# Optimization experiments

Measured on AMD Instinct MI355X. Metric: run time of the kernel, lower is better.

The kernel has to match this reference:

```python
import jax, jax.numpy as jnp
import numpy as np

D_MODEL = 2048
N_HEADS = 16
N_KV = 8
HEAD_DIM = 128
G = N_HEADS // N_KV  # q heads per kv head
SCALE = float(np.sqrt(HEAD_DIM))
B, T = 2, 2048


def setup_inputs() -> dict:
    key = jax.random.key(0)
    k1, k2, k3, k4, k5 = jax.random.split(key, 5)
    s = 0.02
    return {
        "x": jax.random.normal(k1, (B, T, D_MODEL), dtype=jnp.float32),
        "Wq": jax.random.normal(k2, (N_HEADS * HEAD_DIM, D_MODEL), dtype=jnp.float32) * s,
        "Wk": jax.random.normal(k3, (N_KV * HEAD_DIM, D_MODEL), dtype=jnp.float32) * s,
        "Wv": jax.random.normal(k4, (N_KV * HEAD_DIM, D_MODEL), dtype=jnp.float32) * s,
        "Wo": jax.random.normal(k5, (D_MODEL, N_HEADS * HEAD_DIM), dtype=jnp.float32) * s,
    }


def reference(x, Wq, Wk, Wv, Wo):
    # Projections (nn.Linear: y = x @ W.T), dropout prob = 0 so omitted.
    b, t, _ = x.shape
    q = (x @ Wq.T).reshape(b, t, N_KV, G, HEAD_DIM)   # (B,T,Hkv,G,d)
    k = (x @ Wk.T).reshape(b, t, N_KV, HEAD_DIM)      # (B,T,Hkv,d)
    v = (x @ Wv.T).reshape(b, t, N_KV, HEAD_DIM)
    # GQA: each kv head shared by G query heads (equivalent to repeat_interleave).
    scores = jnp.einsum('btghd,bsgd->bghts', q, k) / SCALE  # (B,Hkv,G,T,T)
    attn = jax.nn.softmax(scores, axis=-1)
    out = jnp.einsum('bghts,bsgd->btghd', attn, v)          # (B,T,Hkv,G,d)
    out = out.reshape(b, t, N_HEADS * HEAD_DIM)
    return out @ Wo.T
```

## Files before the change

### kernel.cpp

```cpp
#include <hip/hip_runtime.h>
#include <hip/hip_bf16.h>

typedef __attribute__((ext_vector_type(8))) short short8;
typedef __attribute__((ext_vector_type(4))) float floatx4;

__device__ inline unsigned short f2bf(float f) {
    unsigned int u = __float_as_uint(f);
    u += 0x7fffu + ((u >> 16) & 1u);
    return (unsigned short)(u >> 16);
}

__device__ inline unsigned int pk_bf16(float lo, float hi) {
    __hip_bfloat162 h = __float22bfloat162_rn(float2{lo, hi});
    unsigned int u;
    __builtin_memcpy(&u, &h, 4);
    return u;
}

__global__ void cast_all_kernel(const float* __restrict__ x,
                                const float* __restrict__ wq,
                                const float* __restrict__ wk,
                                const float* __restrict__ wv,
                                const float* __restrict__ wo,
                                unsigned short* __restrict__ xb,
                                unsigned short* __restrict__ wqkb,
                                unsigned short* __restrict__ wvb,
                                unsigned short* __restrict__ wob) {
    const float C2 = 0.08838834764831845f * 1.4426950408889634f;
    int bid = blockIdx.x;
    const float* src;
    unsigned short* dst;
    int base;
    float sc = 1.0f;
    if (bid < 8192)       { src = x;  dst = xb;             base = bid; }
    else if (bid < 12288) { src = wq; dst = wqkb;           base = bid - 8192; sc = C2; }
    else if (bid < 14336) { src = wk; dst = wqkb + 4194304; base = bid - 12288; }
    else if (bid < 16384) { src = wv; dst = wvb;            base = bid - 14336; }
    else                  { src = wo; dst = wob;            base = bid - 16384; }
    int i = base * 256 + threadIdx.x;
    float4 v = ((const float4*)src)[i];
    ushort4 o;
    o.x = f2bf(v.x * sc); o.y = f2bf(v.y * sc);
    o.z = f2bf(v.z * sc); o.w = f2bf(v.w * sc);
    ((ushort4*)dst)[i] = o;
}

template <int OUT_BF16>
__device__ __forceinline__ void gemm256_body(
        const unsigned short* __restrict__ A,
        const unsigned short* __restrict__ B,
        void* __restrict__ Cp, int ldc, int m0, int n0,
        unsigned short* sL) {
    const int tid  = threadIdx.x;
    const int wave = tid >> 6;
    const int lane = tid & 63;
    const int l16  = lane & 15;
    const int lq   = lane >> 4;
    const int wm   = (wave >> 2) * 128;
    const int wn   = (wave & 3) * 64;
    const int kx   = lq ^ (l16 & 3);

    floatx4 acc[8][4] = {};

    const unsigned short* gA[2];
    const unsigned short* gB[2];
#pragma unroll
    for (int i = 0; i < 2; i++) {
        int c   = wave * 2 + i;
        int row = c * 16 + (lane >> 2);
        int g   = (lane & 3) ^ (row & 3);
        gA[i] = A + (size_t)(m0 + row) * 2048 + g * 8;
        gB[i] = B + (size_t)(n0 + row) * 2048 + g * 8;
    }

#define STG_A32(slot)                                                          \
    do {                                                                       \
        _Pragma("unroll")                                                      \
        for (int i = 0; i < 2; i++) {                                          \
            __builtin_amdgcn_global_load_lds(                                  \
                (const __attribute__((address_space(1))) void*)gA[i],          \
                (__attribute__((address_space(3))) void*)(sL + (slot) * 16384 +\
                                                          (wave * 2 + i) * 512),\
                16, 0, 0);                                                     \
            gA[i] += 32;                                                       \
        }                                                                      \
    } while (0)
#define STG_B32(slot)                                                          \
    do {                                                                       \
        _Pragma("unroll")                                                      \
        for (int i = 0; i < 2; i++) {                                          \
            __builtin_amdgcn_global_load_lds(                                  \
                (const __attribute__((address_space(1))) void*)gB[i],          \
                (__attribute__((address_space(3))) void*)(sL + (slot) * 16384 +\
                                                  8192 + (wave * 2 + i) * 512),\
                16, 0, 0);                                                     \
            gB[i] += 32;                                                       \
        }                                                                      \
    } while (0)

    STG_A32(0); STG_B32(0);
    STG_A32(1); STG_B32(1);

    for (int t = 0; t < 64; t++) {
        const int sc = t & 3;
        const int sn = (t + 2) & 3;
        if (t < 63) asm volatile("s_waitcnt vmcnt(4)" ::: "memory");
        else        asm volatile("s_waitcnt vmcnt(0)" ::: "memory");
        __builtin_amdgcn_s_barrier();
        asm volatile("" ::: "memory");

        const unsigned short* sAc = sL + sc * 16384;
        const unsigned short* sBc = sAc + 8192;
        short8 af[4], bf[4];

#pragma unroll
        for (int mb = 0; mb < 4; mb++)
            af[mb] = *(const short8*)(sAc + (wm + mb * 16 + l16) * 32 + kx * 8);
#pragma unroll
        for (int nb = 0; nb < 4; nb++)
            bf[nb] = *(const short8*)(sBc + (wn + nb * 16 + l16) * 32 + kx * 8);
        if (t < 62) STG_A32(sn);
        __builtin_amdgcn_s_barrier();
        asm volatile("s_waitcnt lgkmcnt(0)" ::: "memory");
        __builtin_amdgcn_sched_barrier(0);
        __builtin_amdgcn_s_setprio(1);
#pragma unroll
        for (int mb = 0; mb < 4; mb++)
#pragma unroll
            for (int nb = 0; nb < 4; nb++)
                acc[mb][nb] = __builtin_amdgcn_mfma_f32_16x16x32_bf16(
                    af[mb], bf[nb], acc[mb][nb], 0, 0, 0);
        __builtin_amdgcn_s_setprio(0);
        __builtin_amdgcn_s_barrier();
        asm volatile("" ::: "memory");

#pragma unroll
        for (int mb = 0; mb < 4; mb++)
            af[mb] = *(const short8*)(sAc + (wm + 64 + mb * 16 + l16) * 32 + kx * 8);
        if (t < 62) STG_B32(sn);
        __builtin_amdgcn_s_barrier();
        asm volatile("s_waitcnt lgkmcnt(0)" ::: "memory");
        __builtin_amdgcn_sched_barrier(0);
        __builtin_amdgcn_s_setprio(1);
#pragma unroll
        for (int mb = 0; mb < 4; mb++)
#pragma unroll
            for (int nb = 0; nb < 4; nb++)
                acc[4 + mb][nb] = __builtin_amdgcn_mfma_f32_16x16x32_bf16(
                    af[mb], bf[nb], acc[4 + mb][nb], 0, 0, 0);
        __builtin_amdgcn_s_setprio(0);
    }
#undef STG_A32
#undef STG_B32

#pragma unroll
    for (int mb = 0; mb < 8; mb++)
#pragma unroll
        for (int nb = 0; nb < 4; nb++)
#pragma unroll
            for (int r = 0; r < 4; r++) {
                int row = m0 + wm + mb * 16 + lq * 4 + r;
                int col = n0 + wn + nb * 16 + l16;
                if (OUT_BF16)
                    ((unsigned short*)Cp)[(size_t)row * ldc + col] = f2bf(acc[mb][nb][r]);
                else
                    ((float*)Cp)[(size_t)row * ldc + col] = acc[mb][nb][r];
            }
}

__global__ __launch_bounds__(512, 1) void gemm_qkv_kernel(
        const unsigned short* __restrict__ x_bf,
        const unsigned short* __restrict__ Wqk,
        const unsigned short* __restrict__ Wv,
        unsigned short* __restrict__ QKb,
        unsigned short* __restrict__ Vtb) {
    __shared__ __align__(16) unsigned short sL[4 * 16384];
    const int bid = blockIdx.x;
    if (bid < 192) {
        gemm256_body<1>(x_bf, Wqk, QKb, 3072,
                        (bid / 12) * 256, (bid % 12) * 256, sL);
    } else {
        int t = bid - 192;
        gemm256_body<1>(Wv, x_bf, Vtb, 4096,
                        (t / 16) * 256, (t % 16) * 256, sL);
    }
}

template <int OUT_BF16>
__device__ __forceinline__ void gemm_bt64_body(
        const unsigned short* __restrict__ A,
        const unsigned short* __restrict__ B,
        void* __restrict__ Cp, int K, int ldc, int m0, int n0,
        unsigned short* sA, unsigned short* sB) {
    const int tid  = threadIdx.x;
    const int wave = tid >> 6;
    const int lane = tid & 63;
    const int l16  = lane & 15;
    const int lq   = lane >> 4;
    const int wm   = (wave >> 1) * 64;
    const int wn   = (wave & 1) * 64;

    floatx4 acc[4][4] = {};

    const unsigned short* gA[4];
    const unsigned short* gB[4];
#pragma unroll
    for (int i = 0; i < 4; i++) {
        int c   = wave * 4 + i;
        int row = c * 8 + (lane >> 3);
        int chs = (lane & 7) ^ (row & 7);
        gA[i] = A + (size_t)(m0 + row) * K + chs * 8;
        gB[i] = B + (size_t)(n0 + row) * K + chs * 8;
    }

    for (int k0 = 0; k0 < K; k0 += 64) {
        __syncthreads();
#pragma unroll
        for (int i = 0; i < 4; i++) {
            int c = wave * 4 + i;
            __builtin_amdgcn_global_load_lds(
                (const __attribute__((address_space(1))) void*)gA[i],
                (__attribute__((address_space(3))) void*)(sA + c * 512), 16, 0, 0);
            gA[i] += 64;
            __builtin_amdgcn_global_load_lds(
                (const __attribute__((address_space(1))) void*)gB[i],
                (__attribute__((address_space(3))) void*)(sB + c * 512), 16, 0, 0);
            gB[i] += 64;
        }
        __syncthreads();

        short8 af[2][4], bfr[2][4];
#pragma unroll
        for (int ks = 0; ks < 2; ks++) {
            int slot = (ks * 4 + lq) ^ (l16 & 7);
#pragma unroll
            for (int mb = 0; mb < 4; mb++)
                af[ks][mb] = *(const short8*)(sA + (wm + mb * 16 + l16) * 64 + slot * 8);
#pragma unroll
            for (int nb = 0; nb < 4; nb++)
                bfr[ks][nb] = *(const short8*)(sB + (wn + nb * 16 + l16) * 64 + slot * 8);
        }
#pragma unroll
        for (int ks = 0; ks < 2; ks++)
#pragma unroll
            for (int mb = 0; mb < 4; mb++)
#pragma unroll
                for (int nb = 0; nb < 4; nb++)
                    acc[mb][nb] = __builtin_amdgcn_mfma_f32_16x16x32_bf16(
                        af[ks][mb], bfr[ks][nb], acc[mb][nb], 0, 0, 0);
    }

#pragma unroll
    for (int mb = 0; mb < 4; mb++)
#pragma unroll
        for (int nb = 0; nb < 4; nb++)
#pragma unroll
            for (int r = 0; r < 4; r++) {
                int row = m0 + wm + mb * 16 + lq * 4 + r;
                int col = n0 + wn + nb * 16 + l16;
                if (OUT_BF16)
                    ((unsigned short*)Cp)[(size_t)row * ldc + col] = f2bf(acc[mb][nb][r]);
                else
                    ((float*)Cp)[(size_t)row * ldc + col] = acc[mb][nb][r];
            }
}

__global__ __launch_bounds__(256) void gemm_o_kernel(
        const unsigned short* __restrict__ A,
        const unsigned short* __restrict__ B,
        float* __restrict__ C) {
    __shared__ __align__(16) unsigned short sA[128 * 64];
    __shared__ __align__(16) unsigned short sB[128 * 64];
    gemm_bt64_body<0>(A, B, C, 2048, 2048,
                      blockIdx.y * 128, blockIdx.x * 128, sA, sB);
}

__global__ __launch_bounds__(256, 2) void flash_kernel(
        const unsigned short* __restrict__ QK,
        const unsigned short* __restrict__ Vt,
        unsigned short* __restrict__ O) {
    __shared__ __align__(16) unsigned short smem[40960];

    const int tid  = threadIdx.x;
    const int wave = tid >> 6;
    const int lane = tid & 63;
    const int l16  = lane & 15;
    const int lq   = lane >> 4;
    const int qt   = blockIdx.x;
    const int bh   = blockIdx.y;
    const int b    = bh >> 4;
    const int h    = bh & 15;
    const int kvh  = h >> 1;
    const size_t tokbase = (size_t)b * 2048 + qt * 128 + wave * 32;

    short8 qf[2][4];
#pragma unroll
    for (int qb = 0; qb < 2; qb++) {
        const unsigned short* qp =
            QK + (tokbase + qb * 16 + l16) * 3072 + h * 128 + lq * 8;
#pragma unroll
        for (int c = 0; c < 4; c++) qf[qb][c] = *(const short8*)(qp + c * 32);
    }

    const unsigned short* gKe =
        QK + ((size_t)b * 2048 + wave * 16 + lq) * 3072 + 2048 + kvh * 128 +
        (l16 ^ lq) * 8;
    const unsigned short* gKo =
        QK + ((size_t)b * 2048 + wave * 16 + 4 + lq) * 3072 + 2048 + kvh * 128 +
        (l16 ^ (lq + 4)) * 8;
    const unsigned short* gV0 =
        Vt + (size_t)(kvh * 128 + wave * 32 + (lane >> 3)) * 4096 +
        (size_t)b * 2048 + ((lane & 7) ^ (lane >> 3)) * 8;

#define STAGE_KT(sKd, sVd)                                                     \
    do {                                                                       \
        _Pragma("unroll")                                                      \
        for (int i = 0; i < 4; i++) {                                          \
            const unsigned short* gk =                                         \
                ((i & 1) ? gKo : gKe) + (i >> 1) * 24576;                      \
            __builtin_amdgcn_global_load_lds(                                  \
                (const __attribute__((address_space(1))) void*)gk,             \
                (__attribute__((address_space(3))) void*)((sKd) +              \
                                                          (wave * 4 + i) * 512),\
                16, 0, 0);                                                     \
            __builtin_amdgcn_global_load_lds(                                  \
                (const __attribute__((address_space(1))) void*)(gV0 +          \
                                                               i * 32768),     \
                (__attribute__((address_space(3))) void*)((sVd) +              \
                                                          (wave * 4 + i) * 512),\
                16, 0, 0);                                                     \
        }                                                                      \
        gKe += 196608; gKo += 196608; gV0 += 64;                               \
    } while (0)

    unsigned short* pB = smem + 32768 + wave * 2048;

    floatx4 oacc[2][8] = {};
    float l_run[2] = {0.0f, 0.0f};

    STAGE_KT(smem, smem + 16384);
    asm volatile("s_waitcnt vmcnt(0)" ::: "memory");
    __builtin_amdgcn_s_barrier();
    asm volatile("" ::: "memory");

    for (int kt = 0; kt < 32; kt++) {
        const int cur = kt & 1;
        const unsigned short* sKc = smem + cur * 8192;
        const unsigned short* sVc = smem + 16384 + cur * 8192;
        if (kt < 31) {
            unsigned short* sKn = smem + (cur ^ 1) * 8192;
            unsigned short* sVn = smem + 16384 + (cur ^ 1) * 8192;
            STAGE_KT(sKn, sVn);
        }

#pragma unroll
        for (int kb = 0; kb < 2; kb++) {
            floatx4 sacc[2] = {};
#pragma unroll
            for (int c = 0; c < 4; c++) {
                short8 kf = *(const short8*)(
                    sKc + (kb * 16 + l16) * 128 + (((c * 4 + lq) ^ (l16 & 7)) * 8));
#pragma unroll
                for (int qb = 0; qb < 2; qb++)
                    sacc[qb] = __builtin_amdgcn_mfma_f32_16x16x32_bf16(
                        kf, qf[qb][c], sacc[qb], 0, 0, 0);
            }
#pragma unroll
            for (int qb = 0; qb < 2; qb++) {
                float p0 = __builtin_exp2f(sacc[qb][0]);
                float p1 = __builtin_exp2f(sacc[qb][1]);
                float p2 = __builtin_exp2f(sacc[qb][2]);
                float p3 = __builtin_exp2f(sacc[qb][3]);
                l_run[qb] += (p0 + p1) + (p2 + p3);
                int row = qb * 16 + l16;
                uint2 u;
                u.x = pk_bf16(p0, p1);
                u.y = pk_bf16(p2, p3);
                *(uint2*)(pB + row * 64 +
                          (((kb * 2 + (lq >> 1)) ^ (row & 7)) * 8) +
                          (lq & 1) * 4) = u;
            }
        }
        asm volatile("s_waitcnt lgkmcnt(0)" ::: "memory");

        short8 pf0[2];
#pragma unroll
        for (int qb = 0; qb < 2; qb++) {
            int row = qb * 16 + l16;
            pf0[qb] = *(const short8*)(pB + row * 64 +
                                       ((lq ^ (row & 7)) * 8));
        }

        __builtin_amdgcn_s_setprio(1);
#pragma unroll
        for (int nb = 0; nb < 8; nb++) {
            short8 vf = *(const short8*)(
                sVc + (nb * 16 + l16) * 64 + ((lq ^ (l16 & 7)) * 8));
#pragma unroll
            for (int qb = 0; qb < 2; qb++)
                oacc[qb][nb] = __builtin_amdgcn_mfma_f32_16x16x32_bf16(
                    vf, pf0[qb], oacc[qb][nb], 0, 0, 0);
        }
        __builtin_amdgcn_s_setprio(0);

#pragma unroll
        for (int kb = 2; kb < 4; kb++) {
            floatx4 sacc[2] = {};
#pragma unroll
            for (int c = 0; c < 4; c++) {
                short8 kf = *(const short8*)(
                    sKc + (kb * 16 + l16) * 128 + (((c * 4 + lq) ^ (l16 & 7)) * 8));
#pragma unroll
                for (int qb = 0; qb < 2; qb++)
                    sacc[qb] = __builtin_amdgcn_mfma_f32_16x16x32_bf16(
                        kf, qf[qb][c], sacc[qb], 0, 0, 0);
            }
#pragma unroll
            for (int qb = 0; qb < 2; qb++) {
                float p0 = __builtin_exp2f(sacc[qb][0]);
                float p1 = __builtin_exp2f(sacc[qb][1]);
                float p2 = __builtin_exp2f(sacc[qb][2]);
                float p3 = __builtin_exp2f(sacc[qb][3]);
                l_run[qb] += (p0 + p1) + (p2 + p3);
                int row = qb * 16 + l16;
                uint2 u;
                u.x = pk_bf16(p0, p1);
                u.y = pk_bf16(p2, p3);
                *(uint2*)(pB + row * 64 +
                          (((kb * 2 + (lq >> 1)) ^ (row & 7)) * 8) +
                          (lq & 1) * 4) = u;
            }
        }
        asm volatile("s_waitcnt lgkmcnt(0)" ::: "memory");

        short8 pf1[2];
#pragma unroll
        for (int qb = 0; qb < 2; qb++) {
            int row = qb * 16 + l16;
            pf1[qb] = *(const short8*)(pB + row * 64 +
                                       (((4 + lq) ^ (row & 7)) * 8));
        }

        __builtin_amdgcn_s_setprio(1);
#pragma unroll
        for (int nb = 0; nb < 8; nb++) {
            short8 vf = *(const short8*)(
                sVc + (nb * 16 + l16) * 64 + (((4 + lq) ^ (l16 & 7)) * 8));
#pragma unroll
            for (int qb = 0; qb < 2; qb++)
                oacc[qb][nb] = __builtin_amdgcn_mfma_f32_16x16x32_bf16(
                    vf, pf1[qb], oacc[qb][nb], 0, 0, 0);
        }
        __builtin_amdgcn_s_setprio(0);

        asm volatile("s_waitcnt vmcnt(0)" ::: "memory");
        __builtin_amdgcn_s_barrier();
        asm volatile("" ::: "memory");
    }
#undef STAGE_KT

#pragma unroll
    for (int qb = 0; qb < 2; qb++) {
        float l = l_run[qb];
        l += __shfl_xor(l, 16);
        l += __shfl_xor(l, 32);
        float inv = 1.0f / l;
        size_t row = (tokbase + qb * 16 + l16) * 2048 + h * 128;
#pragma unroll
        for (int nb = 0; nb < 8; nb++) {
            uint2 u;
            u.x = pk_bf16(oacc[qb][nb][0] * inv, oacc[qb][nb][1] * inv);
            u.y = pk_bf16(oacc[qb][nb][2] * inv, oacc[qb][nb][3] * inv);
            *(uint2*)(O + row + nb * 16 + lq * 4) = u;
        }
    }
}

extern "C" void kernel_launch(void* const* d_in, const int* in_sizes, int n_in,
                              void* d_out, int out_size, void* d_ws, size_t ws_size,
                              hipStream_t stream) {
    const float* x  = (const float*)d_in[0];
    const float* Wq = (const float*)d_in[1];
    const float* Wk = (const float*)d_in[2];
    const float* Wv = (const float*)d_in[3];
    const float* Wo = (const float*)d_in[4];

    char* ws = (char*)d_ws;
    unsigned short* x_bf   = (unsigned short*)(ws);
    unsigned short* Wqk_bf = (unsigned short*)(ws + 16777216);
    unsigned short* Wv_bf  = (unsigned short*)(ws + 29360128);
    unsigned short* Wo_bf  = (unsigned short*)(ws + 33554432);
    unsigned short* QKb    = (unsigned short*)(ws + 41943040);
    unsigned short* Vtb    = (unsigned short*)(ws + 67108864);
    unsigned short* Ob     = (unsigned short*)(ws + 75497472);

    cast_all_kernel<<<dim3(20480), 256, 0, stream>>>(
        x, Wq, Wk, Wv, Wo, x_bf, Wqk_bf, Wv_bf, Wo_bf);

    gemm_qkv_kernel<<<dim3(256), 512, 0, stream>>>(x_bf, Wqk_bf, Wv_bf, QKb, Vtb);

    flash_kernel<<<dim3(16, 32), 256, 0, stream>>>(QKb, Vtb, Ob);

    gemm_o_kernel<<<dim3(16, 32), 256, 0, stream>>>(Ob, Wo_bf, (float*)d_out);
}
```

Measured before the change: 316.4 us.

## Rewrite output projection GEMM with 128x256 tiles and 4-stage async LDS pipeline

Replaces the output-projection GEMM body, which was single-buffered with two __syncthreads per 64-wide K step, with a 512-thread 128x256-tile kernel. The new body streams K in chunks of 32 through a 4-slot LDS ring using global_load_lds, issues loads two stages ahead, and waits with explicit vmcnt and s_barrier. It also raises MFMA priority with setprio. The aim is to hide global-load latency and raise MFMA utilisation. The cost is fewer blocks (256) at one block per CU and more intricate synchronisation.

Result: no change. 310.7 us, median of 2 (-1.8%).

```diff
diff --git a/kernel.cpp b/kernel.cpp
--- a/kernel.cpp
+++ b/kernel.cpp
@@ -168,6 +168,106 @@
             }
 }
 
+template <int OUT_BF16>
+__device__ __forceinline__ void gemm128_body(
+        const unsigned short* __restrict__ A,
+        const unsigned short* __restrict__ B,
+        void* __restrict__ Cp, int ldc, int m0, int n0,
+        unsigned short* sL) {
+    const int tid  = threadIdx.x;
+    const int wave = tid >> 6;
+    const int lane = tid & 63;
+    const int l16  = lane & 15;
+    const int lq   = lane >> 4;
+    const int wm   = (wave >> 2) * 64;
+    const int wn   = (wave & 3) * 64;
+    const int kx   = lq ^ (l16 & 3);
+
+    floatx4 acc[4][4] = {};
+
+    const unsigned short* gA0;
+    const unsigned short* gB[2];
+    {
+        int row = wave * 16 + (lane >> 2);
+        int g   = (lane & 3) ^ (row & 3);
+        gA0 = A + (size_t)(m0 + row) * 2048 + g * 8;
+    }
+#pragma unroll
+    for (int i = 0; i < 2; i++) {
+        int c   = wave * 2 + i;
+        int row = c * 16 + (lane >> 2);
+        int g   = (lane & 3) ^ (row & 3);
+        gB[i] = B + (size_t)(n0 + row) * 2048 + g * 8;
+    }
+
+#define STG_O(slot)                                                            \
+    do {                                                                       \
+        __builtin_amdgcn_global_load_lds(                                      \
+            (const __attribute__((address_space(1))) void*)gA0,                \
+            (__attribute__((address_space(3))) void*)(sL + (slot) * 12288 +    \
+                                                      wave * 512),             \
+            16, 0, 0);                                                         \
+        gA0 += 32;                                                             \
+        _Pragma("unroll")                                                      \
+        for (int i = 0; i < 2; i++) {                                          \
+            __builtin_amdgcn_global_load_lds(                                  \
+                (const __attribute__((address_space(1))) void*)gB[i],          \
+                (__attribute__((address_space(3))) void*)(sL + (slot) * 12288 +\
+                                                  4096 + (wave * 2 + i) * 512),\
+                16, 0, 0);                                                     \
+            gB[i] += 32;                                                       \
+        }                                                                      \
+    } while (0)
+
+    STG_O(0); STG_O(1);
+
+    for (int t = 0; t < 64; t++) {
+        const int sc = t & 3;
+        const int sn = (t + 2) & 3;
+        if (t < 63) asm volatile("s_waitcnt vmcnt(3)" ::: "memory");
+        else        asm volatile("s_waitcnt vmcnt(0)" ::: "memory");
+        __builtin_amdgcn_s_barrier();
+        asm volatile("" ::: "memory");
+
+        const unsigned short* sAc = sL + sc * 12288;
+        const unsigned short* sBc = sAc + 4096;
+        short8 af[4], bf[4];
+#pragma unroll
+        for (int mb = 0; mb < 4; mb++)
+            af[mb] = *(const short8*)(sAc + (wm + mb * 16 + l16) * 32 + kx * 8);
+#pragma unroll
+        for (int nb = 0; nb < 4; nb++)
+            bf[nb] = *(const short8*)(sBc + (wn + nb * 16 + l16) * 32 + kx * 8);
+        if (t < 62) STG_O(sn);
+        __builtin_amdgcn_s_barrier();
+        asm volatile("s_waitcnt lgkmcnt(0)" ::: "memory");
+        __builtin_amdgcn_sched_barrier(0);
+        __builtin_amdgcn_s_setprio(1);
+#pragma unroll
+        for (int mb = 0; mb < 4; mb++)
+#pragma unroll
+            for (int nb = 0; nb < 4; nb++)
+                acc[mb][nb] = __builtin_amdgcn_mfma_f32_16x16x32_bf16(
+                    af[mb], bf[nb], acc[mb][nb], 0, 0, 0);
+        __builtin_amdgcn_s_setprio(0);
+    }
+#undef STG_O
+
+#pragma unroll
+    for (int mb = 0; mb < 4; mb++)
+#pragma unroll
+        for (int nb = 0; nb < 4; nb++)
+#pragma unroll
+            for (int r = 0; r < 4; r++) {
+                int row = m0 + wm + mb * 16 + lq * 4 + r;
+                int col = n0 + wn + nb * 16 + l16;
+                if (OUT_BF16)
+                    ((unsigned short*)Cp)[(size_t)row * ldc + col] = f2bf(acc[mb][nb][r]);
+                else
+                    ((float*)Cp)[(size_t)row * ldc + col] = acc[mb][nb][r];
+            }
+}
+
 __global__ __launch_bounds__(512, 1) void gemm_qkv_kernel(
         const unsigned short* __restrict__ x_bf,
         const unsigned short* __restrict__ Wqk,
@@ -186,93 +286,13 @@
     }
 }
 
-template <int OUT_BF16>
-__device__ __forceinline__ void gemm_bt64_body(
-        const unsigned short* __restrict__ A,
-        const unsigned short* __restrict__ B,
-        void* __restrict__ Cp, int K, int ldc, int m0, int n0,
-        unsigned short* sA, unsigned short* sB) {
-    const int tid  = threadIdx.x;
-    const int wave = tid >> 6;
-    const int lane = tid & 63;
-    const int l16  = lane & 15;
-    const int lq   = lane >> 4;
-    const int wm   = (wave >> 1) * 64;
-    const int wn   = (wave & 1) * 64;
-
-    floatx4 acc[4][4] = {};
-
-    const unsigned short* gA[4];
-    const unsigned short* gB[4];
-#pragma unroll
-    for (int i = 0; i < 4; i++) {
-        int c   = wave * 4 + i;
-        int row = c * 8 + (lane >> 3);
-        int chs = (lane & 7) ^ (row & 7);
-        gA[i] = A + (size_t)(m0 + row) * K + chs * 8;
-        gB[i] = B + (size_t)(n0 + row) * K + chs * 8;
-    }
-
-    for (int k0 = 0; k0 < K; k0 += 64) {
-        __syncthreads();
-#pragma unroll
-        for (int i = 0; i < 4; i++) {
-            int c = wave * 4 + i;
-            __builtin_amdgcn_global_load_lds(
-                (const __attribute__((address_space(1))) void*)gA[i],
-                (__attribute__((address_space(3))) void*)(sA + c * 512), 16, 0, 0);
-            gA[i] += 64;
-            __builtin_amdgcn_global_load_lds(
-                (const __attribute__((address_space(1))) void*)gB[i],
-                (__attribute__((address_space(3))) void*)(sB + c * 512), 16, 0, 0);
-            gB[i] += 64;
-        }
-        __syncthreads();
-
-        short8 af[2][4], bfr[2][4];
-#pragma unroll
-        for (int ks = 0; ks < 2; ks++) {
-            int slot = (ks * 4 + lq) ^ (l16 & 7);
-#pragma unroll
-            for (int mb = 0; mb < 4; mb++)
-                af[ks][mb] = *(const short8*)(sA + (wm + mb * 16 + l16) * 64 + slot * 8);
-#pragma unroll
-            for (int nb = 0; nb < 4; nb++)
-                bfr[ks][nb] = *(const short8*)(sB + (wn + nb * 16 + l16) * 64 + slot * 8);
-        }
-#pragma unroll
-        for (int ks = 0; ks < 2; ks++)
-#pragma unroll
-            for (int mb = 0; mb < 4; mb++)
-#pragma unroll
-                for (int nb = 0; nb < 4; nb++)
-                    acc[mb][nb] = __builtin_amdgcn_mfma_f32_16x16x32_bf16(
-                        af[ks][mb], bfr[ks][nb], acc[mb][nb], 0, 0, 0);
-    }
-
-#pragma unroll
-    for (int mb = 0; mb < 4; mb++)
-#pragma unroll
-        for (int nb = 0; nb < 4; nb++)
-#pragma unroll
-            for (int r = 0; r < 4; r++) {
-                int row = m0 + wm + mb * 16 + lq * 4 + r;
-                int col = n0 + wn + nb * 16 + l16;
-                if (OUT_BF16)
-                    ((unsigned short*)Cp)[(size_t)row * ldc + col] = f2bf(acc[mb][nb][r]);
-                else
-                    ((float*)Cp)[(size_t)row * ldc + col] = acc[mb][nb][r];
-            }
-}
-
-__global__ __launch_bounds__(256) void gemm_o_kernel(
+__global__ __launch_bounds__(512, 1) void gemm_o_kernel(
         const unsigned short* __restrict__ A,
         const unsigned short* __restrict__ B,
         float* __restrict__ C) {
-    __shared__ __align__(16) unsigned short sA[128 * 64];
-    __shared__ __align__(16) unsigned short sB[128 * 64];
-    gemm_bt64_body<0>(A, B, C, 2048, 2048,
-                      blockIdx.y * 128, blockIdx.x * 128, sA, sB);
+    __shared__ __align__(16) unsigned short sL[4 * 12288];
+    gemm128_body<0>(A, B, C, 2048,
+                    blockIdx.y * 128, blockIdx.x * 256, sL);
 }
 
 __global__ __launch_bounds__(256, 2) void flash_kernel(
@@ -501,5 +521,5 @@
 
     flash_kernel<<<dim3(16, 32), 256, 0, stream>>>(QKb, Vtb, Ob);
 
-    gemm_o_kernel<<<dim3(16, 32), 256, 0, stream>>>(Ob, Wo_bf, (float*)d_out);
-}
+    gemm_o_kernel<<<dim3(8, 32), 512, 0, stream>>>(Ob, Wo_bf, (float*)d_out);
+}
```
